# Kernel optimization log

Hardware: AMD Instinct MI355X
Metric: run time of the kernel (lower is better)

## Reference

```python
import jax, jax.numpy as jnp
import numpy as np

K = 16  # topK from config


def setup_inputs() -> dict:
    key = jax.random.key(0)
    k1, k2 = jax.random.split(key)
    predictions = jax.random.uniform(k1, (8, 256, 8), dtype=jnp.float32)
    ref_imgs = jax.random.uniform(k2, (8, 3, 192, 192), dtype=jnp.float32)
    return {"predictions": predictions, "ref_imgs": ref_imgs}


def _dist_loss(predictions, ref_imgs):
    bs, L, _ = predictions.shape
    ch, H, W = ref_imgs.shape[1], ref_imgs.shape[2], ref_imgs.shape[3]
    img_size = W  # original uses ref_imgs.shape[-1] for both axes
    pos = predictions[:, :, :2]  # (bs, L, 2), normalized (x, y) in [0, 1]

    # --- nearest grid_sample (align_corners=False, padding zeros) ---
    # Faithful to the original einops mixup: flat sample i uses image i % bs
    # and grid point preds.reshape(bs*L, 2)[i].
    grid = pos.reshape(bs * L, 2)
    img_idx = jnp.arange(bs * L) % bs
    # unnormalize: pix = ((2g - 1) + 1) * S / 2 - 0.5 = g * S - 0.5
    ix = jnp.round(grid[:, 0] * W - 0.5).astype(jnp.int32)
    iy = jnp.round(grid[:, 1] * H - 0.5).astype(jnp.int32)
    inb = ((ix >= 0) & (ix < W) & (iy >= 0) & (iy < H)).astype(ref_imgs.dtype)
    ixc = jnp.clip(ix, 0, W - 1)
    iyc = jnp.clip(iy, 0, H - 1)
    pooled_flat = ref_imgs[img_idx, :, iyc, ixc] * inb[:, None]  # (bs*L, ch)
    # pooled_colors rearranged '(L bs) ch 1 1 -> bs L ch' with flat order (L outer, bs inner)
    pooled = pooled_flat.reshape(L, bs, ch).transpose(1, 0, 2)  # (bs, L, ch)

    # --- per-pixel squared color distance, sum over channels ---
    # ||ref - pooled||^2 = ||ref||^2 - 2<ref, pooled> + ||pooled||^2 (avoids (bs,L,ch,H,W))
    ref_sq = jnp.sum(ref_imgs * ref_imgs, axis=1)  # (bs, H, W)
    cross = jnp.einsum('bchw,blc->blhw', ref_imgs, pooled)  # (bs, L, H, W)
    pooled_sq = jnp.sum(pooled * pooled, axis=-1)  # (bs, L)
    similar = ref_sq[:, None] - 2.0 * cross + pooled_sq[:, :, None, None]

    # --- K most-similar pixel locations ---
    _, idx = jax.lax.top_k(-similar.reshape(bs, L, H * W), K)  # smallest K
    tgt_x = (idx % img_size).astype(pos.dtype) / img_size
    tgt_y = (idx // img_size).astype(pos.dtype) / img_size
    tgt = jnp.stack([tgt_x, tgt_y], axis=-1)  # (bs, L, K, 2)
    tgt_down = jnp.roll(tgt, shift=1, axis=1)

    # --- closest candidate of the previous stroke (positions detached) ---
    pd = jax.lax.stop_gradient(pos)[:, :, None, :]  # (bs, L, 1, 2)
    dist_down = jnp.sum((pd - tgt_down) ** 2, axis=-1)  # (bs, L, K)
    closest = jnp.argmin(dist_down, axis=-1)  # (bs, L)
    final_tgt = jnp.take_along_axis(tgt_down, closest[:, :, None, None], axis=2)[:, :, 0, :]

    loss = jnp.sum((pos[:, 1:] - final_tgt[:, 1:]) ** 2, axis=-1)  # (bs, L-1)
    return jnp.mean(loss)


def reference(predictions, ref_imgs):
    return _dist_loss(predictions, ref_imgs)
```

## Files before the change

### kernel.cpp

```cpp
#include <hip/hip_runtime.h>
#include <stdint.h>

#define BS 8
#define HH 192
#define WW 192
#define HW (HH*WW)
#define KK 16
#define SITES 9216
#define QCAP 512
#define PAD_FILT 4e-5f

typedef unsigned long long u64;


__device__ __forceinline__ uint32_t fkey(float f) {
    uint32_t u = __float_as_uint(f);
    uint32_t mask = (uint32_t)((int32_t)u >> 31) | 0x80000000u;
    return u ^ mask;
}
__device__ __forceinline__ float inv_fkey(uint32_t v) {
    uint32_t u = (v & 0x80000000u) ? (v ^ 0x80000000u) : ~v;
    return __uint_as_float(u);
}

__device__ __forceinline__ u64 umin64(u64 a, u64 b) { return a < b ? a : b; }

__device__ __forceinline__ u64 wave_min_u64(u64 v) {
    #pragma unroll
    for (int off = 32; off >= 1; off >>= 1) {
        uint32_t lo = (uint32_t)v, hi = (uint32_t)(v >> 32);
        lo = __shfl_xor(lo, off, 64);
        hi = __shfl_xor(hi, off, 64);
        u64 o = ((u64)hi << 32) | lo;
        v = umin64(v, o);
    }
    return v;
}

__device__ __forceinline__ void insert64(u64 (&kept)[KK], u64 key) {
    #pragma unroll
    for (int j = KK - 1; j >= 1; --j) {
        u64 a = kept[j - 1];
        u64 mn = umin64(kept[j], key);
        kept[j] = (key < a) ? a : mn;
    }
    kept[0] = umin64(kept[0], key);
}

__device__ __forceinline__ void insert4(uint32_t (&k)[4], uint32_t key) {
    #pragma unroll
    for (int j = 3; j >= 1; --j) {
        uint32_t a = k[j - 1];
        uint32_t mn = min(k[j], key);
        k[j] = (key < a) ? a : mn;
    }
    k[0] = min(k[0], key);
}

__device__ __forceinline__ float exact_rsq(float a, float b, float c) {
    return __fadd_rn(__fadd_rn(__fmul_rn(a, a), __fmul_rn(b, b)), __fmul_rn(c, c));
}
__device__ __forceinline__ float exact_sim(float c0, float c1, float c2, float rsq, float4 pq) {
    float cr = __fadd_rn(__fadd_rn(__fmul_rn(c0, pq.x), __fmul_rn(c1, pq.y)), __fmul_rn(c2, pq.z));
    return __fadd_rn(__fsub_rn(rsq, __fmul_rn(2.0f, cr)), pq.w);
}

#define LOSS_STEP(gmv)                                                   \
{                                                                        \
    uint32_t idxv = (uint32_t)(gmv);                                     \
    float tx = (float)(idxv % WW) / 192.0f;                              \
    float ty = (float)(idxv / WW) / 192.0f;                              \
    float ddx = __fsub_rn(px1, tx);                                      \
    float ddy = __fsub_rn(py1, ty);                                      \
    float dd = __fadd_rn(__fmul_rn(ddx, ddx), __fmul_rn(ddy, ddy));      \
    if (dd < dmin) { dmin = dd; btx = tx; bty = ty; }                    \
}

__global__ __launch_bounds__(1024) void fused_kernel(const float* __restrict__ pred,
                                                     const float* __restrict__ ref,
                                                     float* __restrict__ partial) {
    __shared__ uint32_t smem[8][QCAP];
    __shared__ float4 spool[8];
    __shared__ float sh[8];
    __shared__ uint32_t cnt[8];

    int tid  = threadIdx.x;
    int lane = tid & 63;
    int wid  = tid >> 6;
    int b  = blockIdx.x & 7;
    int qg = blockIdx.x >> 3;

    if (tid < 8) {
        int l = qg * 8 + tid;
        int i = l * BS + b;
        int b2 = i >> 8, l2 = i & 255;
        const float* pr = pred + ((b2 * 256 + l2) * 8);
        float x = pr[0], y = pr[1];
        float fx = rintf(__fsub_rn(__fmul_rn(x, 192.0f), 0.5f));
        float fy = rintf(__fsub_rn(__fmul_rn(y, 192.0f), 0.5f));
        int ix = (int)fx, iy = (int)fy;
        int inb = (ix >= 0 && ix < WW && iy >= 0 && iy < HH) ? 1 : 0;
        int ixc = min(max(ix, 0), WW - 1);
        int iyc = min(max(iy, 0), HH - 1);
        float m = (float)inb;
        const float* img = ref + b * 3 * HW + iyc * WW + ixc;
        float p0 = __fmul_rn(img[0], m);
        float p1 = __fmul_rn(img[HW], m);
        float p2 = __fmul_rn(img[2 * HW], m);
        float psq = __fadd_rn(__fadd_rn(__fmul_rn(p0, p0), __fmul_rn(p1, p1)),
                              __fmul_rn(p2, p2));
        spool[tid] = make_float4(p0, p1, p2, psq);
        cnt[tid] = 0;
    }
    __syncthreads();

    const float4* p0g = (const float4*)(ref + (size_t)b * 3 * HW);
    int myq = tid & 7;
    float4 sp = spool[myq];

    uint32_t kept[4] = {~0u, ~0u, ~0u, ~0u};
    {
        int site = tid;
        float4 n0 = p0g[site], n1 = p0g[site + SITES], n2 = p0g[site + 2 * SITES];
        #pragma unroll 1
        for (int it = 0; it < 8; ++it) {
            float4 a0 = n0, a1 = n1, a2 = n2;
            int sn = (it < 7) ? (site + 1024) : site;
            n0 = p0g[sn]; n1 = p0g[sn + SITES]; n2 = p0g[sn + 2 * SITES];
            #define SAMP1(comp)                                                         \
            {                                                                           \
                float nr = -0.5f * fmaf(a2.comp, a2.comp, fmaf(a1.comp, a1.comp,        \
                                  a0.comp * a0.comp));                                  \
                float d  = fmaf(a2.comp, sp.z, fmaf(a1.comp, sp.y,                      \
                               fmaf(a0.comp, sp.x, nr)));                               \
                uint32_t k = fkey(-d);                                                  \
                if (k < kept[3]) insert4(kept, k);                                      \
            }
            SAMP1(x) SAMP1(y) SAMP1(z) SAMP1(w)
            #undef SAMP1
            site = sn;
        }
    }
    {
        int slot = (tid >> 3) * 4;
        smem[myq][slot + 0] = kept[0];
        smem[myq][slot + 1] = kept[1];
        smem[myq][slot + 2] = kept[2];
        smem[myq][slot + 3] = kept[3];
    }
    __syncthreads();

    if (wid < 8) {
        uint32_t vals[8];
        #pragma unroll
        for (int j = 0; j < 8; ++j) vals[j] = smem[wid][j * 64 + lane];
        uint32_t lo = 0x00800000u, hi = 0xFF7FFFFFu;
        #pragma unroll 1
        for (int t = 0; t < 24; ++t) {
            uint32_t mid = lo + ((hi - lo) >> 1);
            int c = 0;
            #pragma unroll
            for (int j = 0; j < 8; ++j) c += (vals[j] <= mid) ? 1 : 0;
            #pragma unroll
            for (int off = 32; off >= 1; off >>= 1) c += __shfl_xor(c, off, 64);
            if (c >= KK) hi = mid; else lo = mid + 1;
        }
        float hval = -inv_fkey(hi) - PAD_FILT;
        if (qg == 31 && wid == 7) hval = 3.0e38f;
        if (lane == 0) sh[wid] = hval;
    }
    __syncthreads();

    float px[8], py[8], pz[8], hh[8];
    #pragma unroll
    for (int q = 0; q < 8; ++q) {
        float4 s = spool[q];
        px[q] = s.x; py[q] = s.y; pz[q] = s.z; hh[q] = sh[q];
    }

    {
        int site = tid;
        float4 n0 = p0g[site], n1 = p0g[site + SITES], n2 = p0g[site + 2 * SITES];
        #pragma unroll 1
        for (int it = 0; it < 9; ++it) {
            float4 a0 = n0, a1 = n1, a2 = n2;
            int sn = (it < 8) ? (site + 1024) : site;
            n0 = p0g[sn]; n1 = p0g[sn + SITES]; n2 = p0g[sn + 2 * SITES];
            int base = site * 4;

            float nrx = -0.5f * fmaf(a2.x, a2.x, fmaf(a1.x, a1.x, a0.x * a0.x));
            float nry = -0.5f * fmaf(a2.y, a2.y, fmaf(a1.y, a1.y, a0.y * a0.y));
            float nrz = -0.5f * fmaf(a2.z, a2.z, fmaf(a1.z, a1.z, a0.z * a0.z));
            float nrw = -0.5f * fmaf(a2.w, a2.w, fmaf(a1.w, a1.w, a0.w * a0.w));

            #pragma unroll
            for (int q = 0; q < 8; ++q) {
                float dx = fmaf(a2.x, pz[q], fmaf(a1.x, py[q], fmaf(a0.x, px[q], nrx)));
                float dy = fmaf(a2.y, pz[q], fmaf(a1.y, py[q], fmaf(a0.y, px[q], nry)));
                float dz = fmaf(a2.z, pz[q], fmaf(a1.z, py[q], fmaf(a0.z, px[q], nrz)));
                float dw = fmaf(a2.w, pz[q], fmaf(a1.w, py[q], fmaf(a0.w, px[q], nrw)));
                bool g0 = dx >= hh[q];
                bool g1 = dy >= hh[q];
                bool g2 = dz >= hh[q];
                bool g3 = dw >= hh[q];
                if (__ballot(g0 | g1 | g2 | g3)) {
                    #define PUSHI(gc, ei)                                          \
                    if (gc) {                                                      \
                        uint32_t slot = atomicAdd(&cnt[q], 1u);                    \
                        if (slot < QCAP) smem[q][slot] = (uint32_t)(base + ei);    \
                    }
                    PUSHI(g0, 0) PUSHI(g1, 1) PUSHI(g2, 2) PUSHI(g3, 3)
                    #undef PUSHI
                }
            }
            site = sn;
        }
    }
    __syncthreads();

    if (wid < 8) {
        int l  = qg * 8 + wid;
        int bl = b * 256 + l;
        if (l == 255) {
            if (lane == 0) partial[bl] = 0.0f;
        } else {
            uint32_t U = cnt[wid];
            float px1 = pred[(size_t)(bl + 1) * 8 + 0];
            float py1 = pred[(size_t)(bl + 1) * 8 + 1];
            float4 pqv = spool[wid];
            const float* rb = ref + (size_t)b * 3 * HW;
            float dmin = 3.4e38f, btx = 0.0f, bty = 0.0f;

            if (U <= QCAP) {
                u64 r0, r1, r2, r3, r4, r5, r6, r7;
                #define LOADJ(jj, rj)                                                   \
                {                                                                       \
                    uint32_t e = (jj) * 64 + lane;                                      \
                    u64 v = ~0ull;                                                      \
                    if (e < U) {                                                        \
                        uint32_t pidx = smem[wid][e];                                   \
                        float c0v = rb[pidx], c1v = rb[pidx + HW], c2v = rb[pidx + 2 * HW]; \
                        float rs = exact_rsq(c0v, c1v, c2v);                            \
                        float sx = exact_sim(c0v, c1v, c2v, rs, pqv);                   \
                        v = ((u64)fkey(sx) << 32) | pidx;                               \
                    }                                                                   \
                    rj = v;                                                             \
                }
                LOADJ(0, r0) LOADJ(1, r1) LOADJ(2, r2) LOADJ(3, r3)
                LOADJ(4, r4) LOADJ(5, r5) LOADJ(6, r6) LOADJ(7, r7)
                #undef LOADJ

                #pragma unroll 1
                for (int rnd = 0; rnd < 16; ++rnd) {
                    u64 mloc = umin64(umin64(umin64(r0, r1), umin64(r2, r3)),
                                      umin64(umin64(r4, r5), umin64(r6, r7)));
                    u64 gm = wave_min_u64(mloc);
                    if (gm != ~0ull) LOSS_STEP(gm)
                    r0 = (r0 == gm) ? ~0ull : r0;
                    r1 = (r1 == gm) ? ~0ull : r1;
                    r2 = (r2 == gm) ? ~0ull : r2;
                    r3 = (r3 == gm) ? ~0ull : r3;
                    r4 = (r4 == gm) ? ~0ull : r4;
                    r5 = (r5 == gm) ? ~0ull : r5;
                    r6 = (r6 == gm) ? ~0ull : r6;
                    r7 = (r7 == gm) ? ~0ull : r7;
                }
            } else {
                u64 kept16[KK];
                #pragma unroll
                for (int j = 0; j < KK; ++j) kept16[j] = ~0ull;
                const float4* pg = (const float4*)rb;
                #pragma unroll 1
                for (int st = lane; st < SITES; st += 64) {
                    float4 a0 = pg[st], a1 = pg[st + SITES], a2 = pg[st + 2 * SITES];
                    int base = st * 4;
                    #define FB(comp, ei)                                                \
                    {                                                                   \
                        float rs = exact_rsq(a0.comp, a1.comp, a2.comp);                \
                        float sx = exact_sim(a0.comp, a1.comp, a2.comp, rs, pqv);       \
                        u64 key = ((u64)fkey(sx) << 32) | (uint32_t)(base + (ei));      \
                        if (key < kept16[KK - 1]) insert64(kept16, key);                \
                    }
                    FB(x, 0) FB(y, 1) FB(z, 2) FB(w, 3)
                    #undef FB
                }
                #pragma unroll 1
                for (int rnd = 0; rnd < 16; ++rnd) {
                    u64 gm = wave_min_u64(kept16[0]);
                    if (kept16[0] == gm) {
                        #pragma unroll
                        for (int j = 0; j < KK - 1; ++j) kept16[j] = kept16[j + 1];
                        kept16[KK - 1] = ~0ull;
                    }
                    LOSS_STEP(gm)
                }
            }

            if (lane == 0) {
                float ex = __fsub_rn(px1, btx);
                float ey = __fsub_rn(py1, bty);
                partial[bl] = __fadd_rn(__fmul_rn(ex, ex), __fmul_rn(ey, ey));
            }
        }
    }
}

__global__ __launch_bounds__(256) void reduce_kernel(const float* __restrict__ partial,
                                                     float* __restrict__ out) {
    __shared__ double sred[256];
    double a = 0.0;
    #pragma unroll
    for (int i = 0; i < 8; ++i) a += (double)partial[i * 256 + threadIdx.x];
    sred[threadIdx.x] = a;
    __syncthreads();
    for (int s = 128; s > 0; s >>= 1) {
        if (threadIdx.x < s) sred[threadIdx.x] += sred[threadIdx.x + s];
        __syncthreads();
    }
    if (threadIdx.x == 0) out[0] = (float)(sred[0] / 2040.0);
}

extern "C" void kernel_launch(void* const* d_in, const int* in_sizes, int n_in,
                              void* d_out, int out_size, void* d_ws, size_t ws_size,
                              hipStream_t stream) {
    const float* pred = (const float*)d_in[0];
    const float* ref  = (const float*)d_in[1];
    float* out = (float*)d_out;

    float* partial = (float*)d_ws;

    fused_kernel <<<256, 1024, 0, stream>>>(pred, ref, partial);
    reduce_kernel<<<  1,  256, 0, stream>>>(partial, out);
}
```

Before: 102.2 us.

## Use per-thread max threshold and ballot-based per-wave candidate segments

Result: no change. 100.2 us (-1.9%).

```diff
diff --git a/kernel.cpp b/kernel.cpp
--- a/kernel.cpp
+++ b/kernel.cpp
@@ -7,7 +7,9 @@
 #define HW (HH*WW)
 #define KK 16
 #define SITES 9216
-#define QCAP 512
+#define NW 16
+#define SEGSZ 64
+#define UCAP 512
 #define PAD_FILT 4e-5f
 
 typedef unsigned long long u64;
@@ -24,6 +26,11 @@
 }
 
 __device__ __forceinline__ u64 umin64(u64 a, u64 b) { return a < b ? a : b; }
+
+__device__ __forceinline__ uint32_t mbcnt64(u64 m) {
+    return __builtin_amdgcn_mbcnt_hi((uint32_t)(m >> 32),
+            __builtin_amdgcn_mbcnt_lo((uint32_t)m, 0));
+}
 
 __device__ __forceinline__ u64 wave_min_u64(u64 v) {
     #pragma unroll
@@ -45,16 +52,6 @@
         kept[j] = (key < a) ? a : mn;
     }
     kept[0] = umin64(kept[0], key);
-}
-
-__device__ __forceinline__ void insert4(uint32_t (&k)[4], uint32_t key) {
-    #pragma unroll
-    for (int j = 3; j >= 1; --j) {
-        uint32_t a = k[j - 1];
-        uint32_t mn = min(k[j], key);
-        k[j] = (key < a) ? a : mn;
-    }
-    k[0] = min(k[0], key);
 }
 
 __device__ __forceinline__ float exact_rsq(float a, float b, float c) {
@@ -79,10 +76,11 @@
 __global__ __launch_bounds__(1024) void fused_kernel(const float* __restrict__ pred,
                                                      const float* __restrict__ ref,
                                                      float* __restrict__ partial) {
-    __shared__ uint32_t smem[8][QCAP];
+    __shared__ uint32_t seg[8 * NW * SEGSZ];
+    __shared__ uint32_t compactb[8 * UCAP];
+    __shared__ uint32_t scnts[8 * NW];
     __shared__ float4 spool[8];
     __shared__ float sh[8];
-    __shared__ uint32_t cnt[8];
 
     int tid  = threadIdx.x;
     int lane = tid & 63;
@@ -110,7 +108,6 @@
         float psq = __fadd_rn(__fadd_rn(__fmul_rn(p0, p0), __fmul_rn(p1, p1)),
                               __fmul_rn(p2, p2));
         spool[tid] = make_float4(p0, p1, p2, psq);
-        cnt[tid] = 0;
     }
     __syncthreads();
 
@@ -118,7 +115,7 @@
     int myq = tid & 7;
     float4 sp = spool[myq];
 
-    uint32_t kept[4] = {~0u, ~0u, ~0u, ~0u};
+    float md = -3.4e38f;
     {
         int site = tid;
         float4 n0 = p0g[site], n1 = p0g[site + SITES], n2 = p0g[site + 2 * SITES];
@@ -127,40 +124,34 @@
             float4 a0 = n0, a1 = n1, a2 = n2;
             int sn = (it < 7) ? (site + 1024) : site;
             n0 = p0g[sn]; n1 = p0g[sn + SITES]; n2 = p0g[sn + 2 * SITES];
-            #define SAMP1(comp)                                                         \
+            #define SAMPM(comp)                                                         \
             {                                                                           \
                 float nr = -0.5f * fmaf(a2.comp, a2.comp, fmaf(a1.comp, a1.comp,        \
                                   a0.comp * a0.comp));                                  \
                 float d  = fmaf(a2.comp, sp.z, fmaf(a1.comp, sp.y,                      \
                                fmaf(a0.comp, sp.x, nr)));                               \
-                uint32_t k = fkey(-d);                                                  \
-                if (k < kept[3]) insert4(kept, k);                                      \
+                md = fmaxf(md, d);                                                      \
             }
-            SAMP1(x) SAMP1(y) SAMP1(z) SAMP1(w)
-            #undef SAMP1
+            SAMPM(x) SAMPM(y) SAMPM(z) SAMPM(w)
+            #undef SAMPM
             site = sn;
         }
     }
-    {
-        int slot = (tid >> 3) * 4;
-        smem[myq][slot + 0] = kept[0];
-        smem[myq][slot + 1] = kept[1];
-        smem[myq][slot + 2] = kept[2];
-        smem[myq][slot + 3] = kept[3];
-    }
+    seg[tid] = fkey(-md);
+
+    int site3 = tid;
+    float4 f0 = p0g[site3], f1 = p0g[site3 + SITES], f2 = p0g[site3 + 2 * SITES];
+
     __syncthreads();
 
     if (wid < 8) {
-        uint32_t vals[8];
-        #pragma unroll
-        for (int j = 0; j < 8; ++j) vals[j] = smem[wid][j * 64 + lane];
+        uint32_t v0 = seg[lane * 8 + wid];
+        uint32_t v1 = seg[(lane + 64) * 8 + wid];
         uint32_t lo = 0x00800000u, hi = 0xFF7FFFFFu;
         #pragma unroll 1
         for (int t = 0; t < 24; ++t) {
             uint32_t mid = lo + ((hi - lo) >> 1);
-            int c = 0;
-            #pragma unroll
-            for (int j = 0; j < 8; ++j) c += (vals[j] <= mid) ? 1 : 0;
+            int c = ((v0 <= mid) ? 1 : 0) + ((v1 <= mid) ? 1 : 0);
             #pragma unroll
             for (int off = 32; off >= 1; off >>= 1) c += __shfl_xor(c, off, 64);
             if (c >= KK) hi = mid; else lo = mid + 1;
@@ -171,50 +162,65 @@
     }
     __syncthreads();
 
-    float px[8], py[8], pz[8], hh[8];
+    float px[8], py[8], pz[8], hq[8];
     #pragma unroll
     for (int q = 0; q < 8; ++q) {
         float4 s = spool[q];
-        px[q] = s.x; py[q] = s.y; pz[q] = s.z; hh[q] = sh[q];
-    }
-
-    {
-        int site = tid;
-        float4 n0 = p0g[site], n1 = p0g[site + SITES], n2 = p0g[site + 2 * SITES];
-        #pragma unroll 1
-        for (int it = 0; it < 9; ++it) {
-            float4 a0 = n0, a1 = n1, a2 = n2;
-            int sn = (it < 8) ? (site + 1024) : site;
-            n0 = p0g[sn]; n1 = p0g[sn + SITES]; n2 = p0g[sn + 2 * SITES];
-            int base = site * 4;
-
-            float nrx = -0.5f * fmaf(a2.x, a2.x, fmaf(a1.x, a1.x, a0.x * a0.x));
-            float nry = -0.5f * fmaf(a2.y, a2.y, fmaf(a1.y, a1.y, a0.y * a0.y));
-            float nrz = -0.5f * fmaf(a2.z, a2.z, fmaf(a1.z, a1.z, a0.z * a0.z));
-            float nrw = -0.5f * fmaf(a2.w, a2.w, fmaf(a1.w, a1.w, a0.w * a0.w));
-
-            #pragma unroll
-            for (int q = 0; q < 8; ++q) {
-                float dx = fmaf(a2.x, pz[q], fmaf(a1.x, py[q], fmaf(a0.x, px[q], nrx)));
-                float dy = fmaf(a2.y, pz[q], fmaf(a1.y, py[q], fmaf(a0.y, px[q], nry)));
-                float dz = fmaf(a2.z, pz[q], fmaf(a1.z, py[q], fmaf(a0.z, px[q], nrz)));
-                float dw = fmaf(a2.w, pz[q], fmaf(a1.w, py[q], fmaf(a0.w, px[q], nrw)));
-                bool g0 = dx >= hh[q];
-                bool g1 = dy >= hh[q];
-                bool g2 = dz >= hh[q];
-                bool g3 = dw >= hh[q];
-                if (__ballot(g0 | g1 | g2 | g3)) {
-                    #define PUSHI(gc, ei)                                          \
-                    if (gc) {                                                      \
-                        uint32_t slot = atomicAdd(&cnt[q], 1u);                    \
-                        if (slot < QCAP) smem[q][slot] = (uint32_t)(base + ei);    \
-                    }
-                    PUSHI(g0, 0) PUSHI(g1, 1) PUSHI(g2, 2) PUSHI(g3, 3)
-                    #undef PUSHI
-                }
-            }
-            site = sn;
+        px[q] = s.x; py[q] = s.y; pz[q] = s.z; hq[q] = sh[q];
+    }
+    uint32_t scq0 = 0, scq1 = 0, scq2 = 0, scq3 = 0,
+             scq4 = 0, scq5 = 0, scq6 = 0, scq7 = 0;
+
+    #pragma unroll 1
+    for (int it = 0; it < 9; ++it) {
+        float4 a0 = f0, a1 = f1, a2 = f2;
+        int sn = (it < 8) ? (site3 + 1024) : site3;
+        f0 = p0g[sn]; f1 = p0g[sn + SITES]; f2 = p0g[sn + 2 * SITES];
+        int base = site3 * 4;
+
+        float nrx = -0.5f * fmaf(a2.x, a2.x, fmaf(a1.x, a1.x, a0.x * a0.x));
+        float nry = -0.5f * fmaf(a2.y, a2.y, fmaf(a1.y, a1.y, a0.y * a0.y));
+        float nrz = -0.5f * fmaf(a2.z, a2.z, fmaf(a1.z, a1.z, a0.z * a0.z));
+        float nrw = -0.5f * fmaf(a2.w, a2.w, fmaf(a1.w, a1.w, a0.w * a0.w));
+
+        #define QPUSH(q, scq)                                                           \
+        {                                                                               \
+            float d0 = fmaf(a2.x, pz[q], fmaf(a1.x, py[q], fmaf(a0.x, px[q], nrx)));    \
+            float d1 = fmaf(a2.y, pz[q], fmaf(a1.y, py[q], fmaf(a0.y, px[q], nry)));    \
+            float d2 = fmaf(a2.z, pz[q], fmaf(a1.z, py[q], fmaf(a0.z, px[q], nrz)));    \
+            float d3 = fmaf(a2.w, pz[q], fmaf(a1.w, py[q], fmaf(a0.w, px[q], nrw)));    \
+            u64 m0 = __ballot(d0 >= hq[q]);                                             \
+            u64 m1 = __ballot(d1 >= hq[q]);                                             \
+            u64 m2 = __ballot(d2 >= hq[q]);                                             \
+            u64 m3 = __ballot(d3 >= hq[q]);                                             \
+            if (m0 | m1 | m2 | m3) {                    \
+                uint32_t sb = ((q) * NW + wid) * SEGSZ;                                 \
+                uint32_t c = scq;                                                       \
+                if (d0 >= hq[q]) { uint32_t s = c + mbcnt64(m0);                        \
+                                   if (s < SEGSZ) seg[sb + s] = (uint32_t)(base + 0); } \
+                c += (uint32_t)__popcll(m0);                                            \
+                if (d1 >= hq[q]) { uint32_t s = c + mbcnt64(m1);                        \
+                                   if (s < SEGSZ) seg[sb + s] = (uint32_t)(base + 1); } \
+                c += (uint32_t)__popcll(m1);                                            \
+                if (d2 >= hq[q]) { uint32_t s = c + mbcnt64(m2);                        \
+                                   if (s < SEGSZ) seg[sb + s] = (uint32_t)(base + 2); } \
+                c += (uint32_t)__popcll(m2);                                            \
+                if (d3 >= hq[q]) { uint32_t s = c + mbcnt64(m3);                        \
+                                   if (s < SEGSZ) seg[sb + s] = (uint32_t)(base + 3); } \
+                c += (uint32_t)__popcll(m3);                                            \
+                scq = c;                                                                \
+            }                                                                           \
         }
+        QPUSH(0, scq0) QPUSH(1, scq1) QPUSH(2, scq2) QPUSH(3, scq3)
+        QPUSH(4, scq4) QPUSH(5, scq5) QPUSH(6, scq6) QPUSH(7, scq7)
+        #undef QPUSH
+        site3 = sn;
+    }
+    if (lane == 0) {
+        scnts[0 * NW + wid] = scq0; scnts[1 * NW + wid] = scq1;
+        scnts[2 * NW + wid] = scq2; scnts[3 * NW + wid] = scq3;
+        scnts[4 * NW + wid] = scq4; scnts[5 * NW + wid] = scq5;
+        scnts[6 * NW + wid] = scq6; scnts[7 * NW + wid] = scq7;
     }
     __syncthreads();
 
@@ -224,21 +230,38 @@
         if (l == 255) {
             if (lane == 0) partial[bl] = 0.0f;
         } else {
-            uint32_t U = cnt[wid];
+            uint32_t cA[16];
+            #pragma unroll
+            for (int j = 0; j < 16; ++j) cA[j] = scnts[wid * NW + j];
+            bool ovf = false;
+            uint32_t pref = 0;
+            #pragma unroll
+            for (int j = 0; j < 16; ++j) {
+                uint32_t c = cA[j];
+                ovf = ovf || (c > SEGSZ);
+                uint32_t cc = min(c, (uint32_t)SEGSZ);
+                if (lane < cc && pref + lane < UCAP)
+                    compactb[wid * UCAP + pref + lane] =
+                        seg[(wid * NW + j) * SEGSZ + lane];
+                pref += cc;
+            }
+            uint32_t U = pref;
+            if (U > UCAP) ovf = true;
+
             float px1 = pred[(size_t)(bl + 1) * 8 + 0];
             float py1 = pred[(size_t)(bl + 1) * 8 + 1];
             float4 pqv = spool[wid];
             const float* rb = ref + (size_t)b * 3 * HW;
             float dmin = 3.4e38f, btx = 0.0f, bty = 0.0f;
 
-            if (U <= QCAP) {
+            if (!ovf) {
                 u64 r0, r1, r2, r3, r4, r5, r6, r7;
                 #define LOADJ(jj, rj)                                                   \
                 {                                                                       \
                     uint32_t e = (jj) * 64 + lane;                                      \
                     u64 v = ~0ull;                                                      \
                     if (e < U) {                                                        \
-                        uint32_t pidx = smem[wid][e];                                   \
+                        uint32_t pidx = compactb[wid * UCAP + e];                       \
                         float c0v = rb[pidx], c1v = rb[pidx + HW], c2v = rb[pidx + 2 * HW]; \
                         float rs = exact_rsq(c0v, c1v, c2v);                            \
                         float sx = exact_sim(c0v, c1v, c2v, rs, pqv);                   \
```
